# Kernel optimization log

Measured on AMD Instinct MI355X. Metric: run time of the kernel, lower is better.

## Reference

```python
import jax, jax.numpy as jnp
import numpy as np

N, G, E = 100000, 32768, 1000000
F, H = 64, 64


def _mlp(x, w1, b1, w2, b2):
    # Linear -> SiLU -> Linear (matches nn.Sequential in the torch module)
    return jax.nn.silu(x @ w1 + b1) @ w2 + b2


def setup_inputs() -> dict:
    key = jax.random.key(0)
    ks = jax.random.split(key, 24)

    def lin(k, fan_in, fan_out):
        s = 1.0 / np.sqrt(fan_in)
        kw, kb = jax.random.split(k)
        w = jax.random.uniform(kw, (fan_in, fan_out), jnp.float32, -s, s)
        b = jax.random.uniform(kb, (fan_out,), jnp.float32, -s, s)
        return w, b

    node_w1, node_b1 = lin(ks[0], F, H)
    node_w2, node_b2 = lin(ks[1], H, H)
    edge_w1, edge_b1 = lin(ks[2], 6, H)
    edge_w2, edge_b2 = lin(ks[3], H, H)
    msg_w1, msg_b1 = lin(ks[4], 2 * H, H)
    msg_w2, msg_b2 = lin(ks[5], H, H)
    upd_w1, upd_b1 = lin(ks[6], H, H)
    upd_w2, upd_b2 = lin(ks[7], H, H)

    return {
        "node_features": jax.random.normal(ks[8], (N, F), jnp.float32),
        "node_pos": jax.random.normal(ks[9], (N, 3), jnp.float32),
        "grid_pos": jax.random.normal(ks[10], (G, 3), jnp.float32),
        "orientations": jax.random.normal(ks[11], (N, 3, 3), jnp.float32),
        "edge_index": jnp.stack([
            jax.random.randint(ks[12], (E,), 0, N),
            jax.random.randint(ks[13], (E,), 0, G),
        ]),
        "node_w1": node_w1, "node_b1": node_b1, "node_w2": node_w2, "node_b2": node_b2,
        "edge_w1": edge_w1, "edge_b1": edge_b1, "edge_w2": edge_w2, "edge_b2": edge_b2,
        "msg_w1": msg_w1, "msg_b1": msg_b1, "msg_w2": msg_w2, "msg_b2": msg_b2,
        "upd_w1": upd_w1, "upd_b1": upd_b1, "upd_w2": upd_w2, "upd_b2": upd_b2,
    }


def reference(node_features, node_pos, grid_pos, orientations, edge_index,
              node_w1, node_b1, node_w2, node_b2,
              edge_w1, edge_b1, edge_w2, edge_b2,
              msg_w1, msg_b1, msg_w2, msg_b2,
              upd_w1, upd_b1, upd_w2, upd_b2):
    source, target = edge_index[0], edge_index[1]
    num_grid = grid_pos.shape[0]

    # node MLP
    h_node = _mlp(node_features, node_w1, node_b1, node_w2, node_b2)  # [N,H]

    # per-edge message with orientation-aware projection
    pos_s = node_pos[source]                 # [E,3]
    rel = grid_pos[target] - pos_s           # [E,3]
    # bmm(rel[:,None,:], R[source]).squeeze(1) == einsum ei,eij->ej
    trel = jnp.einsum("ei,eij->ej", rel, orientations[source])
    edge_attr = jnp.concatenate([pos_s, trel], axis=-1)        # [E,6]
    e_feat = _mlp(edge_attr, edge_w1, edge_b1, edge_w2, edge_b2)
    msg_in = jnp.concatenate([h_node[source], e_feat], axis=-1)  # [E,2H]
    messages = _mlp(msg_in, msg_w1, msg_b1, msg_w2, msg_b2)      # [E,H]

    # scatter-mean into grid buckets (mask out-of-range targets)
    valid = (target >= 0) & (target < num_grid)
    idx = jnp.where(valid, target, 0)
    msg_masked = jnp.where(valid[:, None], messages, 0.0)
    sums = jax.ops.segment_sum(msg_masked, idx, num_segments=num_grid)
    cnts = jax.ops.segment_sum(valid.astype(jnp.float32), idx, num_segments=num_grid)
    grid_feat = sums / jnp.maximum(cnts, 1.0)[:, None]

    return _mlp(grid_feat, upd_w1, upd_b1, upd_w2, upd_b2)  # [G,H]
```

## Files before the change

kernel.cpp:

```cpp
#include <hip/hip_runtime.h>
#include <hip/hip_bf16.h>
#include <cstdint>

typedef __attribute__((ext_vector_type(8))) short short8;
typedef __attribute__((ext_vector_type(4))) float f32x4;
typedef unsigned short u16;

__device__ __forceinline__ float b2f(u16 u) {
  union { unsigned int i; float f; } v; v.i = ((unsigned int)u) << 16; return v.f;
}
__device__ __forceinline__ u16 f2b(float f) {
  __hip_bfloat16 h = __float2bfloat16(f);
  union { __hip_bfloat16 h; u16 u; } v; v.h = h; return v.u;
}
__device__ __forceinline__ float silu_f(float x) {
  return x * __builtin_amdgcn_rcpf(1.0f + __expf(-x));
}

__device__ __forceinline__ float loadF(const void* p, long i, int isf32) {
  if (isf32) return ((const float*)p)[i];
  return b2f(((const u16*)p)[i]);
}

__device__ __forceinline__ int sniffbit(u16 u) {
  unsigned e = (u >> 7) & 0xffu;
  return (e >= 0xC0u || (e < 0x40u && (u & 0x7fffu) != 0)) ? 1 : 0;
}

struct Ptrs { const void* p[20]; int n[20]; };

#define FW_EW1 0
#define FW_UW1 384
#define FW_UW2 4480
#define FW_UB1 8576
#define FW_UB2 8640
#define FW_EB1 8704
#define FW_EB2 8768
#define FW_MB1 8832
#define FW_MB2 8896
#define FW_TOTAL 8960

#define IMG_EW2 0
#define IMG_MW1 4608
#define IMG_MW2 13312
#define IMG_TOTAL 17920

#define PREP_BLOCKS 105
#define HIST_BLOCKS 1024

__global__ __launch_bounds__(256) void hist_detect_k(
    Ptrs a, const int* __restrict__ eidx, int* __restrict__ cnt8,
    int* __restrict__ flags, long E, int G)
{
  const int t = threadIdx.x;
  const int b = blockIdx.x;
  if (b < HIST_BLOCKS) {
    int* cs = cnt8 + (size_t)(b & 7) * G;
    long i = (long)b * 256 + t;
    const long stride = (long)HIST_BLOCKS * 256;
    for (; i < E; i += stride) {
      int tg = eidx[E + i];
      if (tg >= 0 && tg < G) atomicAdd(&cs[tg], 1);
    }
    return;
  }
  int j = b - HIST_BLOCKS;
  const u16* q = (const u16*)a.p[j];
  int n = a.n[j];
  int m = n < 4096 ? n : 4096;
  int cnt = 0;
  for (int i = t; i < m; i += 256) cnt += sniffbit(q[i]);
  __shared__ int tot;
  if (t == 0) tot = 0;
  __syncthreads();
  if (cnt) atomicAdd(&tot, cnt);
  __syncthreads();
  if (t == 0) flags[j] = (tot >= 2) ? 1 : 0;
}

__global__ __launch_bounds__(256) void scan_prep_node_k(
    Ptrs a, const int* __restrict__ flags,
    const int* __restrict__ cnt8, int* __restrict__ cursor8,
    int* __restrict__ bsum,
    u16* __restrict__ img, float* __restrict__ fw,
    u16* __restrict__ hout, int nrows, int G, int NB2)
{
  const int t = threadIdx.x;
  const int b = blockIdx.x;

  if (b < NB2) {
    __shared__ int sd[256];
    const long tot = 8L * G;
    long j0 = (long)b * 1024 + (long)t * 4;
    int v[4];
#pragma unroll
    for (int k = 0; k < 4; ++k) {
      long j = j0 + k;
      v[k] = (j < tot) ? cnt8[(size_t)(j & 7) * G + (j >> 3)] : 0;
    }
    int local = v[0] + v[1] + v[2] + v[3];
    sd[t] = local;
    __syncthreads();
    for (int off = 1; off < 256; off <<= 1) {
      int x2 = (t >= off) ? sd[t - off] : 0;
      __syncthreads();
      sd[t] += x2;
      __syncthreads();
    }
    int p = sd[t] - local;
#pragma unroll
    for (int k = 0; k < 4; ++k) {
      long j = j0 + k;
      if (j < tot) cursor8[(size_t)(j & 7) * G + (j >> 3)] = p;
      p += v[k];
    }
    if (t == 255) bsum[b] = sd[255];
    return;
  }

  if (b < NB2 + PREP_BLOCKS) {
    int i = (b - NB2) * 256 + t;
    if (i < IMG_TOTAL) {
      const void* bp; int fl; long si; bool real;
      if (i < IMG_MW1) { int nn = i / 72, k = i % 72; bp = a.p[10]; fl = flags[10]; real = k < 64; si = (long)k * 64 + nn; }
      else if (i < IMG_MW2) { int t2 = i - IMG_MW1; int nn = t2 / 136, k = t2 % 136; bp = a.p[12]; fl = flags[12]; real = k < 128; si = (long)k * 64 + nn; }
      else { int t2 = i - IMG_MW2; int nn = t2 / 72, k = t2 % 72; bp = a.p[14]; fl = flags[14]; real = k < 64; si = (long)k * 64 + nn; }
      u16 val = 0;
      if (real) val = f2b(loadF(bp, si, fl));
      img[i] = val;
    } else if (i < IMG_TOTAL + FW_TOTAL) {
      int j = i - IMG_TOTAL;
      const void* bp; int fl; long si;
      if (j < 384)        { bp = a.p[8];  fl = flags[8];  si = j; }
      else if (j < 4480)  { bp = a.p[16]; fl = flags[16]; si = j - 384; }
      else if (j < 8576)  { bp = a.p[18]; fl = flags[18]; si = j - 4480; }
      else {
        int bb = j - 8576; int seg = bb >> 6; si = bb & 63;
        switch (seg) {
          case 0: bp = a.p[17]; fl = flags[17]; break;
          case 1: bp = a.p[19]; fl = flags[19]; break;
          case 2: bp = a.p[9];  fl = flags[9];  break;
          case 3: bp = a.p[11]; fl = flags[11]; break;
          case 4: bp = a.p[13]; fl = flags[13]; break;
          default: bp = a.p[15]; fl = flags[15]; break;
        }
      }
      fw[j] = loadF(bp, si, fl);
    }
    return;
  }

  __shared__ float xs[64][68];
  __shared__ float w1s[64][68];
  __shared__ float w2s[64][68];
  __shared__ float b1s[64];
  __shared__ float b2s[64];
  const void* x = a.p[0];
  const int xf = flags[0], f1 = flags[4], fb1 = flags[5], f2 = flags[6], fb2 = flags[7];
  const long rbase = (long)(b - NB2 - PREP_BLOCKS) * 64;
  for (int i = t; i < 4096; i += 256) {
    int k = i >> 6, cc = i & 63;
    w1s[k][cc] = loadF(a.p[4], i, f1);
    w2s[k][cc] = loadF(a.p[6], i, f2);
  }
  if (t < 64) { b1s[t] = loadF(a.p[5], t, fb1); b2s[t] = loadF(a.p[7], t, fb2); }
  {
    int row = t >> 2, ch = t & 3;
    long rg = rbase + row;
    if (rg < nrows) {
      if (xf) {
        const float* xp = (const float*)x + rg * 64 + ch * 16;
#pragma unroll
        for (int m = 0; m < 16; ++m) xs[row][ch * 16 + m] = xp[m];
      } else {
        const u16* xp = (const u16*)x + rg * 64 + ch * 16;
#pragma unroll
        for (int m = 0; m < 16; ++m) xs[row][ch * 16 + m] = b2f(xp[m]);
      }
    } else {
#pragma unroll
      for (int m = 0; m < 16; ++m) xs[row][ch * 16 + m] = 0.f;
    }
  }
  __syncthreads();
  const int r0 = (t >> 4) * 4, c0 = (t & 15) * 4;
  float acc[4][4];
#pragma unroll
  for (int i = 0; i < 4; ++i)
#pragma unroll
    for (int j = 0; j < 4; ++j) acc[i][j] = b1s[c0 + j];
  for (int k = 0; k < 64; ++k) {
    float w0 = w1s[k][c0], w1v = w1s[k][c0 + 1], w2v = w1s[k][c0 + 2], w3v = w1s[k][c0 + 3];
#pragma unroll
    for (int i = 0; i < 4; ++i) {
      float av = xs[r0 + i][k];
      acc[i][0] = fmaf(av, w0, acc[i][0]);
      acc[i][1] = fmaf(av, w1v, acc[i][1]);
      acc[i][2] = fmaf(av, w2v, acc[i][2]);
      acc[i][3] = fmaf(av, w3v, acc[i][3]);
    }
  }
  __syncthreads();
#pragma unroll
  for (int i = 0; i < 4; ++i)
#pragma unroll
    for (int j = 0; j < 4; ++j) xs[r0 + i][c0 + j] = silu_f(acc[i][j]);
  __syncthreads();
  float acc2[4][4];
#pragma unroll
  for (int i = 0; i < 4; ++i)
#pragma unroll
    for (int j = 0; j < 4; ++j) acc2[i][j] = b2s[c0 + j];
  for (int k = 0; k < 64; ++k) {
    float w0 = w2s[k][c0], w1v = w2s[k][c0 + 1], w2v = w2s[k][c0 + 2], w3v = w2s[k][c0 + 3];
#pragma unroll
    for (int i = 0; i < 4; ++i) {
      float av = xs[r0 + i][k];
      acc2[i][0] = fmaf(av, w0, acc2[i][0]);
      acc2[i][1] = fmaf(av, w1v, acc2[i][1]);
      acc2[i][2] = fmaf(av, w2v, acc2[i][2]);
      acc2[i][3] = fmaf(av, w3v, acc2[i][3]);
    }
  }
#pragma unroll
  for (int i = 0; i < 4; ++i) {
    long rg = rbase + r0 + i;
    if (rg < nrows) {
#pragma unroll
      for (int j = 0; j < 4; ++j) hout[rg * 64 + c0 + j] = f2b(acc2[i][j]);
    }
  }
}

__global__ __launch_bounds__(256) void scat_k(const int* __restrict__ eidx,
                                              int* __restrict__ cursor8,
                                              const int* __restrict__ bsum,
                                              unsigned int* __restrict__ pkS,
                                              int* __restrict__ evp,
                                              long E, int G, int NB2) {
  __shared__ int bo[256];
  const int t = threadIdx.x;
  int v = (t < NB2) ? bsum[t] : 0;
  bo[t] = v;
  __syncthreads();
  for (int off = 1; off < 256; off <<= 1) {
    int x2 = (t >= off) ? bo[t - off] : 0;
    __syncthreads();
    bo[t] += x2;
    __syncthreads();
  }
  if (blockIdx.x == 0 && t == 0) *evp = bo[NB2 - 1];
  int excl = bo[t] - v;
  __syncthreads();
  bo[t] = excl;
  __syncthreads();
  const int c = blockIdx.x & 7;
  int* cur = cursor8 + (size_t)c * G;
  long i = (long)blockIdx.x * 256 + t;
  const long stride = (long)gridDim.x * 256;
  for (; i < E; i += stride) {
    int tg = eidx[E + i];
    if (tg >= 0 && tg < G) {
      int s = eidx[i];
      long j = ((long)tg << 3) | c;
      int p = atomicAdd(&cur[tg], 1) + bo[j >> 10];
      __builtin_nontemporal_store((unsigned int)s | ((unsigned int)tg << 17), pkS + p);
    }
  }
}

#define ETILES 4

__global__ __launch_bounds__(256, 5) void edge_kernel(
    const void* node_pos, const void* grid_pos, const void* orient,
    const unsigned int* __restrict__ pkS, const int* __restrict__ evp,
    const u16* __restrict__ h_node, const u16* __restrict__ img,
    const float* __restrict__ fw, const int* __restrict__ flags,
    float* __restrict__ sums, int G)
{
  __shared__ __align__(16) u16 pool[4][2304];
  __shared__ float w1e[6][64];
  __shared__ float biasE[4][64];

  const int t = threadIdx.x;
  const int pf = flags[1], gf = flags[2], of = flags[3];
  const int Ev = *evp;

  const int lane = t & 63, w = t >> 6;
  const int q = lane >> 4, c = lane & 15;
  const int m0 = w * 16;
  u16 (* __restrict__ efeat)[72] = (u16 (*)[72])&pool[w][0];
  u16 (* __restrict__ ef1w)[72]  = (u16 (*)[72])&pool[w][1152];
  float (* __restrict__ msgfw)[66] = (float (*)[66])&pool[w][0];
  const u16* wE2 = img + IMG_EW2;
  const u16* wM1 = img + IMG_MW1;
  const u16* wM2 = img + IMG_MW2;
  const f32x4 z = {0.f, 0.f, 0.f, 0.f};

  const long blockBase = (long)blockIdx.x * (ETILES * 64);

  unsigned int pkA = 0, pkB = 0, pkC = 0, pkD = 0;
  if (lane < 16) {
    long e0 = blockBase + m0 + lane;
    if (e0 < Ev)       pkA = pkS[e0];
    if (e0 + 64 < Ev)  pkB = pkS[e0 + 64];
    if (e0 + 128 < Ev) pkC = pkS[e0 + 128];
    if (e0 + 192 < Ev) pkD = pkS[e0 + 192];
  }

  short8 hv0, hv1;
  int ptg, ntg;

  {
    unsigned int pks = (unsigned int)__shfl((int)pkA, c);
    int ss = (int)(pks & 0x1FFFFu);
    const u16* hp = h_node + (long)ss * 64 + q * 8;
    hv0 = *(const short8*)hp;
    hv1 = *(const short8*)(hp + 32);
    long gPrev = blockBase + m0 - 1;
    long gNext = blockBase + m0 + 16;
    ptg = (gPrev >= 0 && gPrev < Ev) ? (int)(pkS[gPrev] >> 17) : -2;
    ntg = (gNext < Ev) ? (int)(pkS[gNext] >> 17) : -2;
  }

  for (int i = t; i < 384; i += 256) w1e[i / 64][i % 64] = fw[FW_EW1 + i];
  { int seg = t >> 6, cc = t & 63; biasE[seg][cc] = fw[FW_EB1 + seg * 64 + cc]; }
  __syncthreads();

  for (int tile = 0; tile < ETILES; ++tile) {
    long base = blockBase + (long)tile * 64;
    if (base >= Ev) break;

    int mytg = -1;
    short8 a0e, a1e;
    {
      float ps0 = 0.f, ps1 = 0.f, ps2 = 0.f, tr0 = 0.f, tr1 = 0.f, tr2 = 0.f;
      if (lane < 16) {
        long eg = base + m0 + lane;
        int gs = (int)(pkA & 0x1FFFFu);
        mytg = (eg < Ev) ? (int)(pkA >> 17) : -1;
        int tgc = (mytg >= 0) ? mytg : 0;
        ps0 = loadF(node_pos, (long)gs * 3 + 0, pf);
        ps1 = loadF(node_pos, (long)gs * 3 + 1, pf);
        ps2 = loadF(node_pos, (long)gs * 3 + 2, pf);
        float rel0 = loadF(grid_pos, (long)tgc * 3 + 0, gf) - ps0;
        float rel1 = loadF(grid_pos, (long)tgc * 3 + 1, gf) - ps1;
        float rel2 = loadF(grid_pos, (long)tgc * 3 + 2, gf) - ps2;
        float o0 = loadF(orient, (long)gs * 9 + 0, of);
        float o1 = loadF(orient, (long)gs * 9 + 1, of);
        float o2 = loadF(orient, (long)gs * 9 + 2, of);
        float o3 = loadF(orient, (long)gs * 9 + 3, of);
        float o4 = loadF(orient, (long)gs * 9 + 4, of);
        float o5 = loadF(orient, (long)gs * 9 + 5, of);
        float o6 = loadF(orient, (long)gs * 9 + 6, of);
        float o7 = loadF(orient, (long)gs * 9 + 7, of);
        float o8 = loadF(orient, (long)gs * 9 + 8, of);
        tr0 = rel0 * o0; tr0 = fmaf(rel1, o3, tr0); tr0 = fmaf(rel2, o6, tr0);
        tr1 = rel0 * o1; tr1 = fmaf(rel1, o4, tr1); tr1 = fmaf(rel2, o7, tr1);
        tr2 = rel0 * o2; tr2 = fmaf(rel1, o5, tr2); tr2 = fmaf(rel2, o8, tr2);
      }
      float a0 = __shfl(ps0, c), a1 = __shfl(ps1, c), a2 = __shfl(ps2, c);
      float a3 = __shfl(tr0, c), a4 = __shfl(tr1, c), a5 = __shfl(tr2, c);
      __align__(16) u16 tA[8], tB[8];
#pragma unroll
      for (int jj = 0; jj < 8; ++jj) {
        int colA = q * 8 + jj;
        int colB = 32 + q * 8 + jj;
        float accA = biasE[0][colA];
        accA = fmaf(a0, w1e[0][colA], accA);
        accA = fmaf(a1, w1e[1][colA], accA);
        accA = fmaf(a2, w1e[2][colA], accA);
        accA = fmaf(a3, w1e[3][colA], accA);
        accA = fmaf(a4, w1e[4][colA], accA);
        accA = fmaf(a5, w1e[5][colA], accA);
        tA[jj] = f2b(silu_f(accA));
        float accB = biasE[0][colB];
        accB = fmaf(a0, w1e[0][colB], accB);
        accB = fmaf(a1, w1e[1][colB], accB);
        accB = fmaf(a2, w1e[2][colB], accB);
        accB = fmaf(a3, w1e[3][colB], accB);
        accB = fmaf(a4, w1e[4][colB], accB);
        accB = fmaf(a5, w1e[5][colB], accB);
        tB[jj] = f2b(silu_f(accB));
      }
      a0e = *(const short8*)tA;
      a1e = *(const short8*)tB;
    }
    {
#pragma unroll
      for (int nt = 0; nt < 4; ++nt) {
        short8 b0 = *(const short8*)&wE2[(nt * 16 + c) * 72 + q * 8];
        short8 b1v = *(const short8*)&wE2[(nt * 16 + c) * 72 + 32 + q * 8];
        f32x4 acc = __builtin_amdgcn_mfma_f32_16x16x32_bf16(a0e, b0, z, 0, 0, 0);
        acc = __builtin_amdgcn_mfma_f32_16x16x32_bf16(a1e, b1v, acc, 0, 0, 0);
#pragma unroll
        for (int r = 0; r < 4; ++r) {
          int row = q * 4 + r, col = nt * 16 + c;
          efeat[row][col] = f2b(acc[r] + biasE[1][col]);
        }
      }
    }
    __builtin_amdgcn_wave_barrier();
    {
      short8 a2 = *(const short8*)&efeat[c][q * 8];
      short8 a3 = *(const short8*)&efeat[c][32 + q * 8];
#pragma unroll
      for (int nt = 0; nt < 4; ++nt) {
        const u16* wp = &wM1[(nt * 16 + c) * 136];
        f32x4 acc = __builtin_amdgcn_mfma_f32_16x16x32_bf16(hv0, *(const short8*)(wp + q * 8), z, 0, 0, 0);
        acc = __builtin_amdgcn_mfma_f32_16x16x32_bf16(hv1, *(const short8*)(wp + 32 + q * 8), acc, 0, 0, 0);
        acc = __builtin_amdgcn_mfma_f32_16x16x32_bf16(a2, *(const short8*)(wp + 64 + q * 8), acc, 0, 0, 0);
        acc = __builtin_amdgcn_mfma_f32_16x16x32_bf16(a3, *(const short8*)(wp + 96 + q * 8), acc, 0, 0, 0);
#pragma unroll
        for (int r = 0; r < 4; ++r) {
          int row = q * 4 + r, col = nt * 16 + c;
          ef1w[row][col] = f2b(silu_f(acc[r] + biasE[2][col]));
        }
      }
    }
    __builtin_amdgcn_wave_barrier();
    {
      short8 a0 = *(const short8*)&ef1w[c][q * 8];
      short8 a1 = *(const short8*)&ef1w[c][32 + q * 8];
      __builtin_amdgcn_wave_barrier();
#pragma unroll
      for (int nt = 0; nt < 4; ++nt) {
        short8 b0 = *(const short8*)&wM2[(nt * 16 + c) * 72 + q * 8];
        short8 b1v = *(const short8*)&wM2[(nt * 16 + c) * 72 + 32 + q * 8];
        f32x4 acc = __builtin_amdgcn_mfma_f32_16x16x32_bf16(a0, b0, z, 0, 0, 0);
        acc = __builtin_amdgcn_mfma_f32_16x16x32_bf16(a1, b1v, acc, 0, 0, 0);
#pragma unroll
        for (int r = 0; r < 4; ++r) {
          int row = q * 4 + r, col = nt * 16 + c;
          msgfw[row][col] = acc[r] + biasE[3][col];
        }
      }
    }
    __builtin_amdgcn_wave_barrier();

    __builtin_amdgcn_sched_barrier(0);
    if (tile + 1 < ETILES && base + 64 < Ev) {
      unsigned int pks2 = (unsigned int)__shfl((int)pkB, c);
      int ss2 = (int)(pks2 & 0x1FFFFu);
      const u16* hp2 = h_node + (long)ss2 * 64 + q * 8;
      hv0 = *(const short8*)hp2;
      hv1 = *(const short8*)(hp2 + 32);
    }
    __builtin_amdgcn_sched_barrier(0);

    {
      int col = lane;
      int cur = __shfl(mytg, 0);
      float run = msgfw[0][col];
      bool lopen = (ptg == cur);
#pragma unroll
      for (int r2 = 1; r2 < 16; ++r2) {
        int tg = __shfl(mytg, r2);
        float v = msgfw[r2][col];
        if (tg == cur) {
          run += v;
        } else {
          if (cur >= 0) {
            if (lopen) unsafeAtomicAdd(&sums[(long)cur * 64 + col], run);
            else sums[(long)cur * 64 + col] = run;
          }
          cur = tg; run = v; lopen = false;
        }
      }
      bool ropen = (ntg == cur);
      if (cur >= 0) {
        if (lopen || ropen) unsafeAtomicAdd(&sums[(long)cur * 64 + col], run);
        else sums[(long)cur * 64 + col] = run;
      }
    }
    __builtin_amdgcn_wave_barrier();

    if (tile + 1 < ETILES && base + 64 < Ev) {
      long gPrev = base + 64 + m0 - 1;
      long gNext = base + 64 + m0 + 16;
      ptg = (gPrev < Ev) ? (int)(pkS[gPrev] >> 17) : -2;
      ntg = (gNext < Ev) ? (int)(pkS[gNext] >> 17) : -2;
    }
    pkA = pkB; pkB = pkC; pkC = pkD;
  }
}

__global__ __launch_bounds__(256) void upd_mlp(
    const float* __restrict__ sums, const int* __restrict__ cnt8,
    const float* __restrict__ fw, float* __restrict__ out, int nrows)
{
  __shared__ float xs[64][68];
  __shared__ float w1s[64][68];
  __shared__ float w2s[64][68];
  __shared__ float b1s[64];
  __shared__ float b2s[64];
  const int t = threadIdx.x;
  const long rbase = (long)blockIdx.x * 64;
  for (int i = t; i < 4096; i += 256) {
    int k = i >> 6, cc = i & 63;
    w1s[k][cc] = fw[FW_UW1 + i];
    w2s[k][cc] = fw[FW_UW2 + i];
  }
  if (t < 64) { b1s[t] = fw[FW_UB1 + t]; b2s[t] = fw[FW_UB2 + t]; }
  {
    int row = t >> 2, ch = t & 3;
    long rg = rbase + row;
    if (rg < nrows) {
      int cn = 0;
#pragma unroll
      for (int cc = 0; cc < 8; ++cc) cn += cnt8[(size_t)cc * nrows + rg];
      float inv = 1.0f / fmaxf((float)cn, 1.0f);
      const float* p = sums + rg * 64 + ch * 16;
#pragma unroll
      for (int m = 0; m < 16; ++m) xs[row][ch * 16 + m] = p[m] * inv;
    } else {
#pragma unroll
      for (int m = 0; m < 16; ++m) xs[row][ch * 16 + m] = 0.f;
    }
  }
  __syncthreads();
  const int r0 = (t >> 4) * 4, c0 = (t & 15) * 4;
  float acc[4][4];
#pragma unroll
  for (int i = 0; i < 4; ++i)
#pragma unroll
    for (int j = 0; j < 4; ++j) acc[i][j] = b1s[c0 + j];
  for (int k = 0; k < 64; ++k) {
    float w0 = w1s[k][c0], w1v = w1s[k][c0 + 1], w2v = w1s[k][c0 + 2], w3v = w1s[k][c0 + 3];
#pragma unroll
    for (int i = 0; i < 4; ++i) {
      float av = xs[r0 + i][k];
      acc[i][0] = fmaf(av, w0, acc[i][0]);
      acc[i][1] = fmaf(av, w1v, acc[i][1]);
      acc[i][2] = fmaf(av, w2v, acc[i][2]);
      acc[i][3] = fmaf(av, w3v, acc[i][3]);
    }
  }
  __syncthreads();
#pragma unroll
  for (int i = 0; i < 4; ++i)
#pragma unroll
    for (int j = 0; j < 4; ++j) xs[r0 + i][c0 + j] = silu_f(acc[i][j]);
  __syncthreads();
  float acc2[4][4];
#pragma unroll
  for (int i = 0; i < 4; ++i)
#pragma unroll
    for (int j = 0; j < 4; ++j) acc2[i][j] = b2s[c0 + j];
  for (int k = 0; k < 64; ++k) {
    float w0 = w2s[k][c0], w1v = w2s[k][c0 + 1], w2v = w2s[k][c0 + 2], w3v = w2s[k][c0 + 3];
#pragma unroll
    for (int i = 0; i < 4; ++i) {
      float av = xs[r0 + i][k];
      acc2[i][0] = fmaf(av, w0, acc2[i][0]);
      acc2[i][1] = fmaf(av, w1v, acc2[i][1]);
      acc2[i][2] = fmaf(av, w2v, acc2[i][2]);
      acc2[i][3] = fmaf(av, w3v, acc2[i][3]);
    }
  }
#pragma unroll
  for (int i = 0; i < 4; ++i) {
    long rg = rbase + r0 + i;
    if (rg < nrows) {
#pragma unroll
      for (int j = 0; j < 4; ++j) out[rg * 64 + c0 + j] = acc2[i][j];
    }
  }
}

extern "C" void kernel_launch(void* const* d_in, const int* in_sizes, int n_in,
                              void* d_out, int out_size, void* d_ws, size_t ws_size,
                              hipStream_t stream) {
  const int N = in_sizes[1] / 3;
  const int G = in_sizes[2] / 3;
  const long E = (long)in_sizes[4] / 2;
  const int NB2 = (int)((8L * G + 1023) / 1024);
  const int nodeBlocks = (N + 63) / 64;

  char* ws = (char*)d_ws;
  float* sums = (float*)ws;
  size_t off = (size_t)G * 256;
  int* cnt8 = (int*)(ws + off);     off += (size_t)G * 32;
  int* cursor8 = (int*)(ws + off);  off += (size_t)G * 32;
  int* bsum = (int*)(ws + off);     off += 1024;
  int* evp = (int*)(ws + off);      off += 256;
  int* flags = (int*)(ws + off);    off += 256;
  unsigned int* pkS = (unsigned int*)(ws + off); off += (size_t)E * 4;
  u16* h_node = (u16*)(ws + off);   off += (size_t)N * 128;
  u16* img = (u16*)(ws + off);      off += (size_t)IMG_TOTAL * 2;
  float* fw = (float*)(ws + off);

  hipMemsetAsync(ws, 0, (size_t)G * 288, stream);

  Ptrs a;
  const int map[20] = {0,1,2,3, 5,6,7,8, 9,10,11,12, 13,14,15,16, 17,18,19,20};
  for (int i = 0; i < 20; ++i) { a.p[i] = d_in[map[i]]; a.n[i] = in_sizes[map[i]]; }

  hist_detect_k<<<HIST_BLOCKS + 20, 256, 0, stream>>>(
      a, (const int*)d_in[4], cnt8, flags, E, G);
  scan_prep_node_k<<<NB2 + PREP_BLOCKS + nodeBlocks, 256, 0, stream>>>(
      a, flags, cnt8, cursor8, bsum, img, fw, h_node, N, G, NB2);
  scat_k<<<1024, 256, 0, stream>>>((const int*)d_in[4], cursor8, bsum, pkS, evp, E, G, NB2);
  edge_kernel<<<(int)((E + ETILES * 64 - 1) / (ETILES * 64)), 256, 0, stream>>>(
      d_in[1], d_in[2], d_in[3], pkS, evp, h_node, img, fw, flags, sums, G);
  upd_mlp<<<(G + 63) / 64, 256, 0, stream>>>(sums, cnt8, fw, (float*)d_out, G);
}
```

Measured before the change: 461.8 us.

## Interleave two edge tiles per wave and regroup preprocessing kernels

The edge kernel now processes two 64-edge tiles (A and B) at once per wave, using a doubled LDS pool and interleaved MFMA chains, so independent work can hide latency. Occupancy is lowered from 5 to 4 blocks per SM to make room. Preprocessing is reorganised: dtype detection moves to its own small kernel, the histogram is fused with weight prep and the node MLP, and the scan becomes a separate kernel. The cost is higher register and LDS pressure and an extra kernel launch.

```diff
diff --git a/kernel.cpp b/kernel.cpp
--- a/kernel.cpp
+++ b/kernel.cpp
@@ -48,12 +48,32 @@
 #define PREP_BLOCKS 105
 #define HIST_BLOCKS 1024
 
-__global__ __launch_bounds__(256) void hist_detect_k(
+__global__ __launch_bounds__(256) void detect_k(Ptrs a, int* __restrict__ flags)
+{
+  const int t = threadIdx.x;
+  const int j = blockIdx.x;
+  const u16* q = (const u16*)a.p[j];
+  int n = a.n[j];
+  int m = n < 4096 ? n : 4096;
+  int cnt = 0;
+  for (int i = t; i < m; i += 256) cnt += sniffbit(q[i]);
+  __shared__ int tot;
+  if (t == 0) tot = 0;
+  __syncthreads();
+  if (cnt) atomicAdd(&tot, cnt);
+  __syncthreads();
+  if (t == 0) flags[j] = (tot >= 2) ? 1 : 0;
+}
+
+__global__ __launch_bounds__(256) void fused_hist_prep_node_k(
     Ptrs a, const int* __restrict__ eidx, int* __restrict__ cnt8,
-    int* __restrict__ flags, long E, int G)
+    const int* __restrict__ flags,
+    u16* __restrict__ img, float* __restrict__ fw,
+    u16* __restrict__ hout, int nrows, int G, long E)
 {
   const int t = threadIdx.x;
   const int b = blockIdx.x;
+
   if (b < HIST_BLOCKS) {
     int* cs = cnt8 + (size_t)(b & 7) * G;
     long i = (long)b * 256 + t;
@@ -64,62 +84,9 @@
     }
     return;
   }
-  int j = b - HIST_BLOCKS;
-  const u16* q = (const u16*)a.p[j];
-  int n = a.n[j];
-  int m = n < 4096 ? n : 4096;
-  int cnt = 0;
-  for (int i = t; i < m; i += 256) cnt += sniffbit(q[i]);
-  __shared__ int tot;
-  if (t == 0) tot = 0;
-  __syncthreads();
-  if (cnt) atomicAdd(&tot, cnt);
-  __syncthreads();
-  if (t == 0) flags[j] = (tot >= 2) ? 1 : 0;
-}
-
-__global__ __launch_bounds__(256) void scan_prep_node_k(
-    Ptrs a, const int* __restrict__ flags,
-    const int* __restrict__ cnt8, int* __restrict__ cursor8,
-    int* __restrict__ bsum,
-    u16* __restrict__ img, float* __restrict__ fw,
-    u16* __restrict__ hout, int nrows, int G, int NB2)
-{
-  const int t = threadIdx.x;
-  const int b = blockIdx.x;
-
-  if (b < NB2) {
-    __shared__ int sd[256];
-    const long tot = 8L * G;
-    long j0 = (long)b * 1024 + (long)t * 4;
-    int v[4];
-#pragma unroll
-    for (int k = 0; k < 4; ++k) {
-      long j = j0 + k;
-      v[k] = (j < tot) ? cnt8[(size_t)(j & 7) * G + (j >> 3)] : 0;
-    }
-    int local = v[0] + v[1] + v[2] + v[3];
-    sd[t] = local;
-    __syncthreads();
-    for (int off = 1; off < 256; off <<= 1) {
-      int x2 = (t >= off) ? sd[t - off] : 0;
-      __syncthreads();
-      sd[t] += x2;
-      __syncthreads();
-    }
-    int p = sd[t] - local;
-#pragma unroll
-    for (int k = 0; k < 4; ++k) {
-      long j = j0 + k;
-      if (j < tot) cursor8[(size_t)(j & 7) * G + (j >> 3)] = p;
-      p += v[k];
-    }
-    if (t == 255) bsum[b] = sd[255];
-    return;
-  }
-
-  if (b < NB2 + PREP_BLOCKS) {
-    int i = (b - NB2) * 256 + t;
+
+  if (b < HIST_BLOCKS + PREP_BLOCKS) {
+    int i = (b - HIST_BLOCKS) * 256 + t;
     if (i < IMG_TOTAL) {
       const void* bp; int fl; long si; bool real;
       if (i < IMG_MW1) { int nn = i / 72, k = i % 72; bp = a.p[10]; fl = flags[10]; real = k < 64; si = (long)k * 64 + nn; }
@@ -157,7 +124,7 @@
   __shared__ float b2s[64];
   const void* x = a.p[0];
   const int xf = flags[0], f1 = flags[4], fb1 = flags[5], f2 = flags[6], fb2 = flags[7];
-  const long rbase = (long)(b - NB2 - PREP_BLOCKS) * 64;
+  const long rbase = (long)(b - HIST_BLOCKS - PREP_BLOCKS) * 64;
   for (int i = t; i < 4096; i += 256) {
     int k = i >> 6, cc = i & 63;
     w1s[k][cc] = loadF(a.p[4], i, f1);
@@ -230,6 +197,40 @@
       for (int j = 0; j < 4; ++j) hout[rg * 64 + c0 + j] = f2b(acc2[i][j]);
     }
   }
+}
+
+__global__ __launch_bounds__(256) void scan_k(
+    const int* __restrict__ cnt8, int* __restrict__ cursor8,
+    int* __restrict__ bsum, int G)
+{
+  const int t = threadIdx.x;
+  const int b = blockIdx.x;
+  __shared__ int sd[256];
+  const long tot = 8L * G;
+  long j0 = (long)b * 1024 + (long)t * 4;
+  int v[4];
+#pragma unroll
+  for (int k = 0; k < 4; ++k) {
+    long j = j0 + k;
+    v[k] = (j < tot) ? cnt8[(size_t)(j & 7) * G + (j >> 3)] : 0;
+  }
+  int local = v[0] + v[1] + v[2] + v[3];
+  sd[t] = local;
+  __syncthreads();
+  for (int off = 1; off < 256; off <<= 1) {
+    int x2 = (t >= off) ? sd[t - off] : 0;
+    __syncthreads();
+    sd[t] += x2;
+    __syncthreads();
+  }
+  int p = sd[t] - local;
+#pragma unroll
+  for (int k = 0; k < 4; ++k) {
+    long j = j0 + k;
+    if (j < tot) cursor8[(size_t)(j & 7) * G + (j >> 3)] = p;
+    p += v[k];
+  }
+  if (t == 255) bsum[b] = sd[255];
 }
 
 __global__ __launch_bounds__(256) void scat_k(const int* __restrict__ eidx,
@@ -271,14 +272,14 @@
 
 #define ETILES 4
 
-__global__ __launch_bounds__(256, 5) void edge_kernel(
+__global__ __launch_bounds__(256, 4) void edge_kernel(
     const void* node_pos, const void* grid_pos, const void* orient,
     const unsigned int* __restrict__ pkS, const int* __restrict__ evp,
     const u16* __restrict__ h_node, const u16* __restrict__ img,
     const float* __restrict__ fw, const int* __restrict__ flags,
     float* __restrict__ sums, int G)
 {
-  __shared__ __align__(16) u16 pool[4][2304];
+  __shared__ __align__(16) u16 pool[4][4608];
   __shared__ float w1e[6][64];
   __shared__ float biasE[4][64];
 
@@ -289,9 +290,12 @@
   const int lane = t & 63, w = t >> 6;
   const int q = lane >> 4, c = lane & 15;
   const int m0 = w * 16;
-  u16 (* __restrict__ efeat)[72] = (u16 (*)[72])&pool[w][0];
-  u16 (* __restrict__ ef1w)[72]  = (u16 (*)[72])&pool[w][1152];
-  float (* __restrict__ msgfw)[66] = (float (*)[66])&pool[w][0];
+  u16 (* __restrict__ efeatA)[72] = (u16 (*)[72])&pool[w][0];
+  u16 (* __restrict__ ef1wA)[72]  = (u16 (*)[72])&pool[w][1152];
+  float (* __restrict__ msgfwA)[66] = (float (*)[66])&pool[w][0];
+  u16 (* __restrict__ efeatB)[72] = (u16 (*)[72])&pool[w][2304];
+  u16 (* __restrict__ ef1wB)[72]  = (u16 (*)[72])&pool[w][3456];
+  float (* __restrict__ msgfwB)[66] = (float (*)[66])&pool[w][2304];
   const u16* wE2 = img + IMG_EW2;
   const u16* wM1 = img + IMG_MW1;
   const u16* wM2 = img + IMG_MW2;
@@ -308,155 +312,265 @@
     if (e0 + 192 < Ev) pkD = pkS[e0 + 192];
   }
 
-  short8 hv0, hv1;
-  int ptg, ntg;
-
+  short8 hvA0, hvA1, hvB0, hvB1;
   {
     unsigned int pks = (unsigned int)__shfl((int)pkA, c);
     int ss = (int)(pks & 0x1FFFFu);
     const u16* hp = h_node + (long)ss * 64 + q * 8;
-    hv0 = *(const short8*)hp;
-    hv1 = *(const short8*)(hp + 32);
-    long gPrev = blockBase + m0 - 1;
-    long gNext = blockBase + m0 + 16;
-    ptg = (gPrev >= 0 && gPrev < Ev) ? (int)(pkS[gPrev] >> 17) : -2;
-    ntg = (gNext < Ev) ? (int)(pkS[gNext] >> 17) : -2;
+    hvA0 = *(const short8*)hp;
+    hvA1 = *(const short8*)(hp + 32);
+    unsigned int pks2 = (unsigned int)__shfl((int)pkB, c);
+    int ss2 = (int)(pks2 & 0x1FFFFu);
+    const u16* hp2 = h_node + (long)ss2 * 64 + q * 8;
+    hvB0 = *(const short8*)hp2;
+    hvB1 = *(const short8*)(hp2 + 32);
+  }
+  int ptgA, ntgA, ptgB, ntgB;
+  {
+    long gPrevA = blockBase + m0 - 1;
+    long gNextA = blockBase + m0 + 16;
+    ptgA = (gPrevA >= 0 && gPrevA < Ev) ? (int)(pkS[gPrevA] >> 17) : -2;
+    ntgA = (gNextA < Ev) ? (int)(pkS[gNextA] >> 17) : -2;
+    long gPrevB = blockBase + 64 + m0 - 1;
+    long gNextB = blockBase + 64 + m0 + 16;
+    ptgB = (gPrevB < Ev) ? (int)(pkS[gPrevB] >> 17) : -2;
+    ntgB = (gNextB < Ev) ? (int)(pkS[gNextB] >> 17) : -2;
   }
 
   for (int i = t; i < 384; i += 256) w1e[i / 64][i % 64] = fw[FW_EW1 + i];
   { int seg = t >> 6, cc = t & 63; biasE[seg][cc] = fw[FW_EB1 + seg * 64 + cc]; }
   __syncthreads();
 
-  for (int tile = 0; tile < ETILES; ++tile) {
-    long base = blockBase + (long)tile * 64;
-    if (base >= Ev) break;
-
-    int mytg = -1;
-    short8 a0e, a1e;
+  for (int p = 0; p < 2; ++p) {
+    long baseA = blockBase + (long)p * 128;
+    if (baseA >= Ev) break;
+    long baseB = baseA + 64;
+    bool doB = (baseB < Ev);
+
+    int mytgA = -1, mytgB = -1;
+    short8 a0eA, a1eA, a0eB, a1eB;
+
     {
-      float ps0 = 0.f, ps1 = 0.f, ps2 = 0.f, tr0 = 0.f, tr1 = 0.f, tr2 = 0.f;
+      float psA0 = 0.f, psA1 = 0.f, psA2 = 0.f, trA0 = 0.f, trA1 = 0.f, trA2 = 0.f;
+      float psB0 = 0.f, psB1 = 0.f, psB2 = 0.f, trB0 = 0.f, trB1 = 0.f, trB2 = 0.f;
       if (lane < 16) {
-        long eg = base + m0 + lane;
-        int gs = (int)(pkA & 0x1FFFFu);
-        mytg = (eg < Ev) ? (int)(pkA >> 17) : -1;
-        int tgc = (mytg >= 0) ? mytg : 0;
-        ps0 = loadF(node_pos, (long)gs * 3 + 0, pf);
-        ps1 = loadF(node_pos, (long)gs * 3 + 1, pf);
-        ps2 = loadF(node_pos, (long)gs * 3 + 2, pf);
-        float rel0 = loadF(grid_pos, (long)tgc * 3 + 0, gf) - ps0;
-        float rel1 = loadF(grid_pos, (long)tgc * 3 + 1, gf) - ps1;
-        float rel2 = loadF(grid_pos, (long)tgc * 3 + 2, gf) - ps2;
-        float o0 = loadF(orient, (long)gs * 9 + 0, of);
-        float o1 = loadF(orient, (long)gs * 9 + 1, of);
-        float o2 = loadF(orient, (long)gs * 9 + 2, of);
-        float o3 = loadF(orient, (long)gs * 9 + 3, of);
-        float o4 = loadF(orient, (long)gs * 9 + 4, of);
-        float o5 = loadF(orient, (long)gs * 9 + 5, of);
-        float o6 = loadF(orient, (long)gs * 9 + 6, of);
-        float o7 = loadF(orient, (long)gs * 9 + 7, of);
-        float o8 = loadF(orient, (long)gs * 9 + 8, of);
-        tr0 = rel0 * o0; tr0 = fmaf(rel1, o3, tr0); tr0 = fmaf(rel2, o6, tr0);
-        tr1 = rel0 * o1; tr1 = fmaf(rel1, o4, tr1); tr1 = fmaf(rel2, o7, tr1);
-        tr2 = rel0 * o2; tr2 = fmaf(rel1, o5, tr2); tr2 = fmaf(rel2, o8, tr2);
-      }
-      float a0 = __shfl(ps0, c), a1 = __shfl(ps1, c), a2 = __shfl(ps2, c);
-      float a3 = __shfl(tr0, c), a4 = __shfl(tr1, c), a5 = __shfl(tr2, c);
-      __align__(16) u16 tA[8], tB[8];
-#pragma unroll
-      for (int jj = 0; jj < 8; ++jj) {
-        int colA = q * 8 + jj;
-        int colB = 32 + q * 8 + jj;
-        float accA = biasE[0][colA];
-        accA = fmaf(a0, w1e[0][colA], accA);
-        accA = fmaf(a1, w1e[1][colA], accA);
-        accA = fmaf(a2, w1e[2][colA], accA);
-        accA = fmaf(a3, w1e[3][colA], accA);
-        accA = fmaf(a4, w1e[4][colA], accA);
-        accA = fmaf(a5, w1e[5][colA], accA);
-        tA[jj] = f2b(silu_f(accA));
-        float accB = biasE[0][colB];
-        accB = fmaf(a0, w1e[0][colB], accB);
-        accB = fmaf(a1, w1e[1][colB], accB);
-        accB = fmaf(a2, w1e[2][colB], accB);
-        accB = fmaf(a3, w1e[3][colB], accB);
-        accB = fmaf(a4, w1e[4][colB], accB);
-        accB = fmaf(a5, w1e[5][colB], accB);
-        tB[jj] = f2b(silu_f(accB));
-      }
-      a0e = *(const short8*)tA;
-      a1e = *(const short8*)tB;
+        int gsA = (int)(pkA & 0x1FFFFu);
+        int tgA = (int)(pkA >> 17);
+        mytgA = (baseA + m0 + lane < Ev) ? tgA : -1;
+        psA0 = loadF(node_pos, (long)gsA * 3 + 0, pf);
+        psA1 = loadF(node_pos, (long)gsA * 3 + 1, pf);
+        psA2 = loadF(node_pos, (long)gsA * 3 + 2, pf);
+        float relA0 = loadF(grid_pos, (long)tgA * 3 + 0, gf) - psA0;
+        float relA1 = loadF(grid_pos, (long)tgA * 3 + 1, gf) - psA1;
+        float relA2 = loadF(grid_pos, (long)tgA * 3 + 2, gf) - psA2;
+        float oA0 = loadF(orient, (long)gsA * 9 + 0, of);
+        float oA1 = loadF(orient, (long)gsA * 9 + 1, of);
+        float oA2 = loadF(orient, (long)gsA * 9 + 2, of);
+        float oA3 = loadF(orient, (long)gsA * 9 + 3, of);
+        float oA4 = loadF(orient, (long)gsA * 9 + 4, of);
+        float oA5 = loadF(orient, (long)gsA * 9 + 5, of);
+        float oA6 = loadF(orient, (long)gsA * 9 + 6, of);
+        float oA7 = loadF(orient, (long)gsA * 9 + 7, of);
+        float oA8 = loadF(orient, (long)gsA * 9 + 8, of);
+        trA0 = relA0 * oA0; trA0 = fmaf(relA1, oA3, trA0); trA0 = fmaf(relA2, oA6, trA0);
+        trA1 = relA0 * oA1; trA1 = fmaf(relA1, oA4, trA1); trA1 = fmaf(relA2, oA7, trA1);
+        trA2 = relA0 * oA2; trA2 = fmaf(relA1, oA5, trA2); trA2 = fmaf(relA2, oA8, trA2);
+        if (doB) {
+          int gsB = (int)(pkB & 0x1FFFFu);
+          int tgB = (int)(pkB >> 17);
+          mytgB = (baseB + m0 + lane < Ev) ? tgB : -1;
+          psB0 = loadF(node_pos, (long)gsB * 3 + 0, pf);
+          psB1 = loadF(node_pos, (long)gsB * 3 + 1, pf);
+          psB2 = loadF(node_pos, (long)gsB * 3 + 2, pf);
+          float relB0 = loadF(grid_pos, (long)tgB * 3 + 0, gf) - psB0;
+          float relB1 = loadF(grid_pos, (long)tgB * 3 + 1, gf) - psB1;
+          float relB2 = loadF(grid_pos, (long)tgB * 3 + 2, gf) - psB2;
+          float oB0 = loadF(orient, (long)gsB * 9 + 0, of);
+          float oB1 = loadF(orient, (long)gsB * 9 + 1, of);
+          float oB2 = loadF(orient, (long)gsB * 9 + 2, of);
+          float oB3 = loadF(orient, (long)gsB * 9 + 3, of);
+          float oB4 = loadF(orient, (long)gsB * 9 + 4, of);
+          float oB5 = loadF(orient, (long)gsB * 9 + 5, of);
+          float oB6 = loadF(orient, (long)gsB * 9 + 6, of);
+          float oB7 = loadF(orient, (long)gsB * 9 + 7, of);
+          float oB8 = loadF(orient, (long)gsB * 9 + 8, of);
+          trB0 = relB0 * oB0; trB0 = fmaf(relB1, oB3, trB0); trB0 = fmaf(relB2, oB6, trB0);
+          trB1 = relB0 * oB1; trB1 = fmaf(relB1, oB4, trB1); trB1 = fmaf(relB2, oB7, trB1);
+          trB2 = relB0 * oB2; trB2 = fmaf(relB1, oB5, trB2); trB2 = fmaf(relB2, oB8, trB2);
+        }
+      }
+      {
+        float a0 = __shfl(psA0, c), a1 = __shfl(psA1, c), a2 = __shfl(psA2, c);
+        float a3 = __shfl(trA0, c), a4 = __shfl(trA1, c), a5 = __shfl(trA2, c);
+        __align__(16) u16 tA[8], tB2[8];
+#pragma unroll
+        for (int jj = 0; jj < 8; ++jj) {
+          int colA = q * 8 + jj;
+          int colB = 32 + q * 8 + jj;
+          float accA = biasE[0][colA];
+          accA = fmaf(a0, w1e[0][colA], accA);
+          accA = fmaf(a1, w1e[1][colA], accA);
+          accA = fmaf(a2, w1e[2][colA], accA);
+          accA = fmaf(a3, w1e[3][colA], accA);
+          accA = fmaf(a4, w1e[4][colA], accA);
+          accA = fmaf(a5, w1e[5][colA], accA);
+          tA[jj] = f2b(silu_f(accA));
+          float accB = biasE[0][colB];
+          accB = fmaf(a0, w1e[0][colB], accB);
+          accB = fmaf(a1, w1e[1][colB], accB);
+          accB = fmaf(a2, w1e[2][colB], accB);
+          accB = fmaf(a3, w1e[3][colB], accB);
+          accB = fmaf(a4, w1e[4][colB], accB);
+          accB = fmaf(a5, w1e[5][colB], accB);
+          tB2[jj] = f2b(silu_f(accB));
+        }
+        a0eA = *(const short8*)tA;
+        a1eA = *(const short8*)tB2;
+      }
+      if (doB) {
+        float a0 = __shfl(psB0, c), a1 = __shfl(psB1, c), a2 = __shfl(psB2, c);
+        float a3 = __shfl(trB0, c), a4 = __shfl(trB1, c), a5 = __shfl(trB2, c);
+        __align__(16) u16 tA[8], tB2[8];
+#pragma unroll
+        for (int jj = 0; jj < 8; ++jj) {
+          int colA = q * 8 + jj;
+          int colB = 32 + q * 8 + jj;
+          float accA = biasE[0][colA];
+          accA = fmaf(a0, w1e[0][colA], accA);
+          accA = fmaf(a1, w1e[1][colA], accA);
+          accA = fmaf(a2, w1e[2][colA], accA);
+          accA = fmaf(a3, w1e[3][colA], accA);
+          accA = fmaf(a4, w1e[4][colA], accA);
+          accA = fmaf(a5, w1e[5][colA], accA);
+          tA[jj] = f2b(silu_f(accA));
+          float accB = biasE[0][colB];
+          accB = fmaf(a0, w1e[0][colB], accB);
+          accB = fmaf(a1, w1e[1][colB], accB);
+          accB = fmaf(a2, w1e[2][colB], accB);
+          accB = fmaf(a3, w1e[3][colB], accB);
+          accB = fmaf(a4, w1e[4][colB], accB);
+          accB = fmaf(a5, w1e[5][colB], accB);
+          tB2[jj] = f2b(silu_f(accB));
+        }
+        a0eB = *(const short8*)tA;
+        a1eB = *(const short8*)tB2;
+      }
     }
     {
 #pragma unroll
       for (int nt = 0; nt < 4; ++nt) {
         short8 b0 = *(const short8*)&wE2[(nt * 16 + c) * 72 + q * 8];
         short8 b1v = *(const short8*)&wE2[(nt * 16 + c) * 72 + 32 + q * 8];
-        f32x4 acc = __builtin_amdgcn_mfma_f32_16x16x32_bf16(a0e, b0, z, 0, 0, 0);
-        acc = __builtin_amdgcn_mfma_f32_16x16x32_bf16(a1e, b1v, acc, 0, 0, 0);
+        f32x4 acc = __builtin_amdgcn_mfma_f32_16x16x32_bf16(a0eA, b0, z, 0, 0, 0);
+        acc = __builtin_amdgcn_mfma_f32_16x16x32_bf16(a1eA, b1v, acc, 0, 0, 0);
 #pragma unroll
         for (int r = 0; r < 4; ++r) {
           int row = q * 4 + r, col = nt * 16 + c;
-          efeat[row][col] = f2b(acc[r] + biasE[1][col]);
+          efeatA[row][col] = f2b(acc[r] + biasE[1][col]);
+        }
+        if (doB) {
+          f32x4 acc2 = __builtin_amdgcn_mfma_f32_16x16x32_bf16(a0eB, b0, z, 0, 0, 0);
+          acc2 = __builtin_amdgcn_mfma_f32_16x16x32_bf16(a1eB, b1v, acc2, 0, 0, 0);
+#pragma unroll
+          for (int r = 0; r < 4; ++r) {
+            int row = q * 4 + r, col = nt * 16 + c;
+            efeatB[row][col] = f2b(acc2[r] + biasE[1][col]);
+          }
         }
       }
     }
     __builtin_amdgcn_wave_barrier();
     {
-      short8 a2 = *(const short8*)&efeat[c][q * 8];
-      short8 a3 = *(const short8*)&efeat[c][32 + q * 8];
+      short8 a2A = *(const short8*)&efeatA[c][q * 8];
+      short8 a3A = *(const short8*)&efeatA[c][32 + q * 8];
 #pragma unroll
       for (int nt = 0; nt < 4; ++nt) {
         const u16* wp = &wM1[(nt * 16 + c) * 136];
-        f32x4 acc = __builtin_amdgcn_mfma_f32_16x16x32_bf16(hv0, *(const short8*)(wp + q * 8), z, 0, 0, 0);
-        acc = __builtin_amdgcn_mfma_f32_16x16x32_bf16(hv1, *(const short8*)(wp + 32 + q * 8), acc, 0, 0, 0);
-        acc = __builtin_amdgcn_mfma_f32_16x16x32_bf16(a2, *(const short8*)(wp + 64 + q * 8), acc, 0, 0, 0);
-        acc = __builtin_amdgcn_mfma_f32_16x16x32_bf16(a3, *(const short8*)(wp + 96 + q * 8), acc, 0, 0, 0);
+        f32x4 acc = __builtin_amdgcn_mfma_f32_16x16x32_bf16(hvA0, *(const short8*)(wp + q * 8), z, 0, 0, 0);
+        acc = __builtin_amdgcn_mfma_f32_16x16x32_bf16(hvA1, *(const short8*)(wp + 32 + q * 8), acc, 0, 0, 0);
+        acc = __builtin_amdgcn_mfma_f32_16x16x32_bf16(a2A, *(const short8*)(wp + 64 + q * 8), acc, 0, 0, 0);
+        acc = __builtin_amdgcn_mfma_f32_16x16x32_bf16(a3A, *(const short8*)(wp + 96 + q * 8), acc, 0, 0, 0);
 #pragma unroll
         for (int r = 0; r < 4; ++r) {
           int row = q * 4 + r, col = nt * 16 + c;
-          ef1w[row][col] = f2b(silu_f(acc[r] + biasE[2][col]));
+          ef1wA[row][col] = f2b(silu_f(acc[r] + biasE[2][col]));
+        }
+      }
+      if (doB) {
+        short8 a2B = *(const short8*)&efeatB[c][q * 8];
+        short8 a3B = *(const short8*)&efeatB[c][32 + q * 8];
+#pragma unroll
+        for (int nt = 0; nt < 4; ++nt) {
+          const u16* wp = &wM1[(nt * 16 + c) * 136];
+          f32x4 acc = __builtin_amdgcn_mfma_f32_16x16x32_bf16(hvB0, *(const short8*)(wp + q * 8), z, 0, 0, 0);
+          acc = __builtin_amdgcn_mfma_f32_16x16x32_bf16(hvB1, *(const short8*)(wp + 32 + q * 8), acc, 0, 0, 0);
+          acc = __builtin_amdgcn_mfma_f32_16x16x32_bf16(a2B, *(const short8*)(wp + 64 + q * 8), acc, 0, 0, 0);
+          acc = __builtin_amdgcn_mfma_f32_16x16x32_bf16(a3B, *(const short8*)(wp + 96 + q * 8), acc, 0, 0, 0);
+#pragma unroll
+          for (int r = 0; r < 4; ++r) {
+            int row = q * 4 + r, col = nt * 16 + c;
+            ef1wB[row][col] = f2b(silu_f(acc[r] + biasE[2][col]));
+          }
         }
       }
     }
     __builtin_amdgcn_wave_barrier();
+
+    if (p == 0 && blockBase + 128 < Ev) {
+      unsigned int pks = (unsigned int)__shfl((int)pkC, c);
+      int ss = (int)(pks & 0x1FFFFu);
+      const u16* hp = h_node + (long)ss * 64 + q * 8;
+      hvA0 = *(const short8*)hp;
+      hvA1 = *(const short8*)(hp + 32);
+      unsigned int pks2 = (unsigned int)__shfl((int)pkD, c);
+      int ss2 = (int)(pks2 & 0x1FFFFu);
+      const u16* hp2 = h_node + (long)ss2 * 64 + q * 8;
+      hvB0 = *(const short8*)hp2;
+      hvB1 = *(const short8*)(hp2 + 32);
+    }
+
     {
-      short8 a0 = *(const short8*)&ef1w[c][q * 8];
-      short8 a1 = *(const short8*)&ef1w[c][32 + q * 8];
+      short8 s4a0A = *(const short8*)&ef1wA[c][q * 8];
+      short8 s4a1A = *(const short8*)&ef1wA[c][32 + q * 8];
+      short8 s4a0B = s4a0A, s4a1B = s4a1A;
+      if (doB) {
+        s4a0B = *(const short8*)&ef1wB[c][q * 8];
+        s4a1B = *(const short8*)&ef1wB[c][32 + q * 8];
+      }
       __builtin_amdgcn_wave_barrier();
 #pragma unroll
       for (int nt = 0; nt < 4; ++nt) {
         short8 b0 = *(const short8*)&wM2[(nt * 16 + c) * 72 + q * 8];
         short8 b1v = *(const short8*)&wM2[(nt * 16 + c) * 72 + 32 + q * 8];
-        f32x4 acc = __builtin_amdgcn_mfma_f32_16x16x32_bf16(a0, b0, z, 0, 0, 0);
-        acc = __builtin_amdgcn_mfma_f32_16x16x32_bf16(a1, b1v, acc, 0, 0, 0);
+        f32x4 acc = __builtin_amdgcn_mfma_f32_16x16x32_bf16(s4a0A, b0, z, 0, 0, 0);
+        acc = __builtin_amdgcn_mfma_f32_16x16x32_bf16(s4a1A, b1v, acc, 0, 0, 0);
 #pragma unroll
         for (int r = 0; r < 4; ++r) {
           int row = q * 4 + r, col = nt * 16 + c;
-          msgfw[row][col] = acc[r] + biasE[3][col];
+          msgfwA[row][col] = acc[r] + biasE[3][col];
+        }
+        if (doB) {
+          f32x4 acc2 = __builtin_amdgcn_mfma_f32_16x16x32_bf16(s4a0B, b0, z, 0, 0, 0);
+          acc2 = __builtin_amdgcn_mfma_f32_16x16x32_bf16(s4a1B, b1v, acc2, 0, 0, 0);
+#pragma unroll
+          for (int r = 0; r < 4; ++r) {
+            int row = q * 4 + r, col = nt * 16 + c;
+            msgfwB[row][col] = acc2[r] + biasE[3][col];
+          }
         }
       }
     }
     __builtin_amdgcn_wave_barrier();
-
-    __builtin_amdgcn_sched_barrier(0);
-    if (tile + 1 < ETILES && base + 64 < Ev) {
-      unsigned int pks2 = (unsigned int)__shfl((int)pkB, c);
-      int ss2 = (int)(pks2 & 0x1FFFFu);
-      const u16* hp2 = h_node + (long)ss2 * 64 + q * 8;
-      hv0 = *(const short8*)hp2;
-      hv1 = *(const short8*)(hp2 + 32);
-    }
-    __builtin_amdgcn_sched_barrier(0);
 
     {
       int col = lane;
-      int cur = __shfl(mytg, 0);
-      float run = msgfw[0][col];
-      bool lopen = (ptg == cur);
+      int cur = __shfl(mytgA, 0);
+      float run = msgfwA[0][col];
+      bool lopen = (ptgA == cur);
 #pragma unroll
       for (int r2 = 1; r2 < 16; ++r2) {
-        int tg = __shfl(mytg, r2);
-        float v = msgfw[r2][col];
+        int tg = __shfl(mytgA, r2);
+        float v = msgfwA[r2][col];
         if (tg == cur) {
           run += v;
         } else {
@@ -467,21 +581,50 @@
           cur = tg; run = v; lopen = false;
         }
       }
-      bool ropen = (ntg == cur);
+      bool ropen = (ntgA == cur);
       if (cur >= 0) {
         if (lopen || ropen) unsafeAtomicAdd(&sums[(long)cur * 64 + col], run);
         else sums[(long)cur * 64 + col] = run;
       }
     }
+    if (doB) {
+      int col = lane;
+      int cur = __shfl(mytgB, 0);
+      float run = msgfwB[0][col];
+      bool lopen = (ptgB == cur);
+#pragma unroll
+      for (int r2 = 1; r2 < 16; ++r2) {
+        int tg = __shfl(mytgB, r2);
+        float v = msgfwB[r2][col];
+        if (tg == cur) {
+          run += v;
+        } else {
+          if (cur >= 0) {
+            if (lopen) unsafeAtomicAdd(&sums[(long)cur * 64 + col], run);
+            else sums[(long)cur * 64 + col] = run;
+          }
+          cur = tg; run = v; lopen = false;
+        }
+      }
+      bool ropen = (ntgB == cur);
+      if (cur >= 0) {
+        if (lopen || ropen) unsafeAtomicAdd(&sums[(long)cur * 64 + col], run);
+        else sums[(long)cur * 64 + col] = run;
+      }
+    }
     __builtin_amdgcn_wave_barrier();
 
-    if (tile + 1 < ETILES && base + 64 < Ev) {
-      long gPrev = base + 64 + m0 - 1;
-      long gNext = base + 64 + m0 + 16;
-      ptg = (gPrev < Ev) ? (int)(pkS[gPrev] >> 17) : -2;
-      ntg = (gNext < Ev) ? (int)(pkS[gNext] >> 17) : -2;
-    }
-    pkA = pkB; pkB = pkC; pkC = pkD;
+    if (p == 0 && blockBase + 128 < Ev) {
+      long gPrevA2 = blockBase + 128 + m0 - 1;
+      long gNextA2 = blockBase + 128 + m0 + 16;
+      ptgA = (gPrevA2 < Ev) ? (int)(pkS[gPrevA2] >> 17) : -2;
+      ntgA = (gNextA2 < Ev) ? (int)(pkS[gNextA2] >> 17) : -2;
+      long gPrevB2 = blockBase + 192 + m0 - 1;
+      long gNextB2 = blockBase + 192 + m0 + 16;
+      ptgB = (gPrevB2 < Ev) ? (int)(pkS[gPrevB2] >> 17) : -2;
+      ntgB = (gNextB2 < Ev) ? (int)(pkS[gNextB2] >> 17) : -2;
+    }
+    pkA = pkC; pkB = pkD;
   }
 }
 
@@ -596,10 +739,10 @@
   const int map[20] = {0,1,2,3, 5,6,7,8, 9,10,11,12, 13,14,15,16, 17,18,19,20};
   for (int i = 0; i < 20; ++i) { a.p[i] = d_in[map[i]]; a.n[i] = in_sizes[map[i]]; }
 
-  hist_detect_k<<<HIST_BLOCKS + 20, 256, 0, stream>>>(
-      a, (const int*)d_in[4], cnt8, flags, E, G);
-  scan_prep_node_k<<<NB2 + PREP_BLOCKS + nodeBlocks, 256, 0, stream>>>(
-      a, flags, cnt8, cursor8, bsum, img, fw, h_node, N, G, NB2);
+  detect_k<<<20, 256, 0, stream>>>(a, flags);
+  fused_hist_prep_node_k<<<HIST_BLOCKS + PREP_BLOCKS + nodeBlocks, 256, 0, stream>>>(
+      a, (const int*)d_in[4], cnt8, flags, img, fw, h_node, N, G, E);
+  scan_k<<<NB2, 256, 0, stream>>>(cnt8, cursor8, bsum, G);
   scat_k<<<1024, 256, 0, stream>>>((const int*)d_in[4], cursor8, bsum, pkS, evp, E, G, NB2);
   edge_kernel<<<(int)((E + ETILES * 64 - 1) / (ETILES * 64)), 256, 0, stream>>>(
       d_in[1], d_in[2], d_in[3], pkS, evp, h_node, img, fw, flags, sums, G);
```

Result: slower. 1.156 ms (+150.3%).
